# Kernel tuning notes

Measured on AMD Instinct MI355X. Metric: run time of the kernel, lower is better.

The kernel has to match this reference:

```python
import jax, jax.numpy as jnp
import numpy as np
import math

D_MODEL = 1024
N_HEAD = 16
D_FF = 4096
B, T, S = 2, 2048, 2048
LN_EPS = 1e-5


def _linear(x, w, b):
    # torch nn.Linear: y = x @ W.T + b, W: [out, in]
    return jnp.einsum('bsd,od->bso', x, w) + b


def _layer_norm(x, g, b):
    mu = jnp.mean(x, axis=-1, keepdims=True)
    var = jnp.var(x, axis=-1, keepdims=True)
    return (x - mu) * jax.lax.rsqrt(var + LN_EPS) * g + b


def _mha(xq, xkv, wq, bq, wk, bk, wv, bv, wo, bo, mask):
    Bq, Tq, D = xq.shape
    Tk = xkv.shape[1]
    dk = D // N_HEAD
    q = _linear(xq, wq, bq).reshape(Bq, Tq, N_HEAD, dk).transpose(0, 2, 1, 3)
    k = _linear(xkv, wk, bk).reshape(Bq, Tk, N_HEAD, dk).transpose(0, 2, 1, 3)
    v = _linear(xkv, wv, bv).reshape(Bq, Tk, N_HEAD, dk).transpose(0, 2, 1, 3)
    scores = jnp.einsum('bhqd,bhkd->bhqk', q, k) / math.sqrt(dk)
    if mask is not None:
        scores = jnp.where(mask == 0, jnp.asarray(-1e9, scores.dtype), scores)
    attn = jax.nn.softmax(scores, axis=-1)  # dropout is eval-mode identity
    out = jnp.einsum('bhqk,bhkd->bhqd', attn, v)
    out = out.transpose(0, 2, 1, 3).reshape(Bq, Tq, D)
    return _linear(out, wo, bo)


def setup_inputs() -> dict:
    key = jax.random.key(0)
    ks = jax.random.split(key, 20)
    sd = 0.02

    def w(k, shape):
        return (jax.random.normal(k, shape, dtype=jnp.float32) * sd)

    inp = {
        'x': jax.random.normal(ks[0], (B, T, D_MODEL), dtype=jnp.float32),
        'enc_output': jax.random.normal(ks[1], (B, S, D_MODEL), dtype=jnp.float32),
        # causal (future) mask for self-attention
        'tgt_mask': jnp.tril(jnp.ones((T, T), dtype=jnp.int32))[None, None, :, :].repeat(B, axis=0),
        # no source padding -> all ones
        'src_tgt_mask': jnp.ones((B, 1, T, S), dtype=jnp.int32),
        'sa_wq': w(ks[2], (D_MODEL, D_MODEL)), 'sa_bq': jnp.zeros((D_MODEL,), jnp.float32),
        'sa_wk': w(ks[3], (D_MODEL, D_MODEL)), 'sa_bk': jnp.zeros((D_MODEL,), jnp.float32),
        'sa_wv': w(ks[4], (D_MODEL, D_MODEL)), 'sa_bv': jnp.zeros((D_MODEL,), jnp.float32),
        'sa_wo': w(ks[5], (D_MODEL, D_MODEL)), 'sa_bo': jnp.zeros((D_MODEL,), jnp.float32),
        'ca_wq': w(ks[6], (D_MODEL, D_MODEL)), 'ca_bq': jnp.zeros((D_MODEL,), jnp.float32),
        'ca_wk': w(ks[7], (D_MODEL, D_MODEL)), 'ca_bk': jnp.zeros((D_MODEL,), jnp.float32),
        'ca_wv': w(ks[8], (D_MODEL, D_MODEL)), 'ca_bv': jnp.zeros((D_MODEL,), jnp.float32),
        'ca_wo': w(ks[9], (D_MODEL, D_MODEL)), 'ca_bo': jnp.zeros((D_MODEL,), jnp.float32),
        'ffn_w1': w(ks[10], (D_FF, D_MODEL)), 'ffn_b1': jnp.zeros((D_FF,), jnp.float32),
        'ffn_w2': w(ks[11], (D_MODEL, D_FF)), 'ffn_b2': jnp.zeros((D_MODEL,), jnp.float32),
        'ln1_g': jnp.ones((D_MODEL,), jnp.float32), 'ln1_b': jnp.zeros((D_MODEL,), jnp.float32),
        'ln2_g': jnp.ones((D_MODEL,), jnp.float32), 'ln2_b': jnp.zeros((D_MODEL,), jnp.float32),
        'ln3_g': jnp.ones((D_MODEL,), jnp.float32), 'ln3_b': jnp.zeros((D_MODEL,), jnp.float32),
    }
    return inp


def reference(x, enc_output, tgt_mask, src_tgt_mask,
              sa_wq, sa_bq, sa_wk, sa_bk, sa_wv, sa_bv, sa_wo, sa_bo,
              ca_wq, ca_bq, ca_wk, ca_bk, ca_wv, ca_bv, ca_wo, ca_bo,
              ffn_w1, ffn_b1, ffn_w2, ffn_b2,
              ln1_g, ln1_b, ln2_g, ln2_b, ln3_g, ln3_b):
    # masked self-attention + residual + LN
    a1 = _mha(x, x, sa_wq, sa_bq, sa_wk, sa_bk, sa_wv, sa_bv, sa_wo, sa_bo, tgt_mask)
    x = _layer_norm(x + a1, ln1_g, ln1_b)
    # cross-attention + residual + LN
    a2 = _mha(x, enc_output, ca_wq, ca_bq, ca_wk, ca_bk, ca_wv, ca_bv, ca_wo, ca_bo, src_tgt_mask)
    x = _layer_norm(x + a2, ln2_g, ln2_b)
    # FFN + residual + LN
    h = jax.nn.relu(_linear(x, ffn_w1, ffn_b1))
    f = _linear(h, ffn_w2, ffn_b2)
    x = _layer_norm(x + f, ln3_g, ln3_b)
    return x
```

## Files before the change

kernel.cpp:

```cpp
#include <hip/hip_runtime.h>
#include <stdint.h>

typedef uint16_t u16;
typedef __attribute__((ext_vector_type(8))) short short8;
typedef __attribute__((ext_vector_type(4))) short short4v;
typedef __attribute__((ext_vector_type(4))) float f32x4;
typedef __attribute__((ext_vector_type(2))) unsigned int u32x2;

#define GLB_AS __attribute__((address_space(1)))
#define LDS_AS __attribute__((address_space(3)))

__device__ __forceinline__ void gload_lds16(const void* g, void* l) {
  __builtin_amdgcn_global_load_lds((GLB_AS void*)(g), (LDS_AS void*)(l), 16, 0, 0);
}

__device__ __forceinline__ float bf2f(u16 u) {
  union { uint32_t i; float f; } v; v.i = ((uint32_t)u) << 16; return v.f;
}
__device__ __forceinline__ u16 f2bf(float f) {
  uint32_t x = __builtin_bit_cast(uint32_t, f);
  return (u16)((x + 0x7fffu + ((x >> 16) & 1u)) >> 16);
}
__device__ __forceinline__ uint32_t cvtpk(float lo, float hi) {
  uint32_t r;
  asm("v_cvt_pk_bf16_f32 %0, %1, %2" : "=v"(r) : "v"(lo), "v"(hi));
  return r;
}

struct CastJobs {
  const float* s[12];
  u16* d[12];
  int n[12];
};
__global__ __launch_bounds__(256) void cast_many(CastJobs j)
{
  const int job = blockIdx.y;
  const int i = (blockIdx.x * 256 + threadIdx.x) * 4;
  if (i >= j.n[job]) return;
  const float4 v = *(const float4*)(j.s[job] + i);
  short4v r;
  r[0] = (short)f2bf(v.x); r[1] = (short)f2bf(v.y);
  r[2] = (short)f2bf(v.z); r[3] = (short)f2bf(v.w);
  *(short4v*)(j.d[job] + i) = r;
}

__global__ __launch_bounds__(256) void vtrans(
    const u16* __restrict__ V, int vs, u16* __restrict__ Vt)
{
  __shared__ u16 tl[64][72];
  const int tid = threadIdx.x;
  const int b = blockIdx.z, h = blockIdx.y, t0 = blockIdx.x * 64;
#pragma unroll
  for (int it = 0; it < 2; ++it) {
    const int r = (tid >> 3) + it*32, c = (tid & 7) * 8;
    short8 vv = *(const short8*)(V + (size_t)(b*2048 + t0 + r)*vs + h*64 + c);
    *(short8*)(&tl[r][c]) = vv;
  }
  __syncthreads();
#pragma unroll
  for (int it = 0; it < 2; ++it) {
    const int d = (tid >> 3) + it*32, t8 = (tid & 7) * 8;
    short8 ov;
#pragma unroll
    for (int j = 0; j < 8; ++j) ov[j] = (short)tl[t8 + j][d];
    *(short8*)(Vt + ((size_t)((b*16 + h)*64 + d))*2048 + t0 + t8) = ov;
  }
}

template<int RELU, int NSEG, int BN>
__global__ __launch_bounds__(256) void gemm_bt(
    const u16* __restrict__ A, const u16* __restrict__ W,
    const float* __restrict__ b0, const float* __restrict__ b1,
    const float* __restrict__ b2, u16* __restrict__ Y,
    int M, int N, int K)
{
  __shared__ __attribute__((aligned(16))) u16 lA[128*64];
  __shared__ __attribute__((aligned(16))) u16 lB[BN*64];
  const int tid  = threadIdx.x;
  const int lane = tid & 63, wv = tid >> 6;
  constexpr int WM = (BN == 128) ? 64 : 32;
  constexpr int MI = WM / 16;
  constexpr int BRND = BN / 32;
  const int wm = (BN == 128) ? (wv >> 1) : wv;
  const int wn = (BN == 128) ? (wv & 1) : 0;
  const int l16 = lane & 15, l4 = lane >> 4;
  const int rswz = (l16 & 7) << 4;

  const int gx = gridDim.x;
  int flat = blockIdx.y * gx + blockIdx.x;
  flat = (flat & 7) * ((gx * gridDim.y) >> 3) + (flat >> 3);
  const int bx = (flat % gx) * BN, by = (flat / gx) * 128;

  const f32x4 fzero = {0.f, 0.f, 0.f, 0.f};
  f32x4 acc[MI][4];
#pragma unroll
  for (int i = 0; i < MI; ++i)
#pragma unroll
    for (int j = 0; j < 4; ++j) acc[i][j] = fzero;

  const int o = wv*1024 + lane*16;
  for (int k0 = 0; k0 < K; k0 += 64) {
#pragma unroll
    for (int r = 0; r < 4; ++r) {
      const int oo = r*4096 + o;
      const int row = oo >> 7;
      const int src = ((oo & 127) ^ ((row & 7) << 4)) >> 1;
      gload_lds16(A + (size_t)(by + row)*K + (k0 + src), (char*)lA + oo);
    }
#pragma unroll
    for (int r = 0; r < BRND; ++r) {
      const int oo = r*4096 + o;
      const int row = oo >> 7;
      const int src = ((oo & 127) ^ ((row & 7) << 4)) >> 1;
      gload_lds16(W + (size_t)(bx + row)*K + (k0 + src), (char*)lB + oo);
    }
    __syncthreads();
#pragma unroll
    for (int ks = 0; ks < 2; ++ks) {
      const int cb = (ks*64 + l4*16) ^ rswz;
      short8 af[MI], bfv[4];
#pragma unroll
      for (int i = 0; i < MI; ++i)
        af[i]  = *(const short8*)((const char*)lA + (wm*WM + i*16 + l16)*128 + cb);
#pragma unroll
      for (int j = 0; j < 4; ++j)
        bfv[j] = *(const short8*)((const char*)lB + (wn*64 + j*16 + l16)*128 + cb);
#pragma unroll
      for (int i = 0; i < MI; ++i)
#pragma unroll
        for (int j = 0; j < 4; ++j)
          acc[i][j] = __builtin_amdgcn_mfma_f32_16x16x32_bf16(af[i], bfv[j], acc[i][j], 0, 0, 0);
    }
    __syncthreads();
  }

#pragma unroll
  for (int j = 0; j < 4; ++j) {
    const int col = bx + wn*64 + j*16 + l16;
    float bv;
    if (NSEG == 1) bv = b0[col];
    else {
      const int seg = col >> 10, off = col & 1023;
      const float* bp = (seg == 0) ? b0 : ((seg == 1) ? b1 : b2);
      bv = bp[off];
    }
#pragma unroll
    for (int i = 0; i < MI; ++i) {
      const int r0 = by + wm*WM + i*16 + l4*4;
#pragma unroll
      for (int r = 0; r < 4; ++r) {
        float v = acc[i][j][r] + bv;
        if (RELU) v = v > 0.f ? v : 0.f;
        Y[(size_t)(r0 + r)*N + col] = f2bf(v);
      }
    }
  }
}

template<int CAUSAL, int QR>
__global__ __launch_bounds__(512, (QR == 16) ? 4 : 2) void attn_fwd(
    const u16* __restrict__ Q, int qs,
    const u16* __restrict__ K, int ks_,
    const u16* __restrict__ Vt, u16* __restrict__ O, int Tk)
{
  constexpr int NG = QR / 16;
  __shared__ __attribute__((aligned(16))) u16 lK[2][128*64];
  __shared__ __attribute__((aligned(16))) u16 lV[2][64*128];
  __shared__ __attribute__((aligned(16))) u16 lP[8][NG*1024];
  const int tid  = threadIdx.x;
  const int lane = tid & 63, wv = tid >> 6;
  const int l16 = lane & 15, l4 = lane >> 4;
  const int b = blockIdx.z, h = blockIdx.y;
  int strip;
  if (CAUSAL) {
    const int u = (blockIdx.x + blockIdx.z) & 15;
    strip = (u & 1) ? (15 - (u >> 1)) : (u >> 1);
  } else {
    strip = blockIdx.x;
  }
  const int Bq = strip * (8 * QR);
  const int qrow = Bq + wv*QR;

  short8 qf[NG][2];
#pragma unroll
  for (int g = 0; g < NG; ++g) {
    const u16* Qb = Q + (size_t)(b*2048 + qrow + g*16 + l16)*qs + h*64;
#pragma unroll
    for (int ks = 0; ks < 2; ++ks)
      qf[g][ks] = *(const short8*)(Qb + ks*32 + l4*8);
  }

  const f32x4 fzero = {0.f, 0.f, 0.f, 0.f};
  f32x4 accO[NG][4];
#pragma unroll
  for (int g = 0; g < NG; ++g)
#pragma unroll
    for (int i = 0; i < 4; ++i) accO[g][i] = fzero;
  float lrow[NG];
#pragma unroll
  for (int g = 0; g < NG; ++g) lrow[g] = 0.f;

  const int kend = CAUSAL ? (Bq + 8*QR) : Tk;
  const int nt = kend >> 7;
  const int qmax = qrow + QR - 1;
  const int srK = tid >> 3;
  const int scK = 8 * ((tid & 7) ^ (srK & 7));
  const int srV = tid >> 4;
  const int scV = 8 * ((tid & 15) ^ (srV & 7));
  const u16* KbG = K  + (size_t)(b*2048)*ks_ + h*64 + scK;
  const u16* VbG = Vt + ((size_t)((b*16 + h)*64 + srV))*2048 + scV;
  const int wvoff = (tid >> 6) * 1024;
  const int rswz = (l16 & 7) << 4;
  const float SCL = 0.18033688f;
  const int sbq = (lane & 48) + l4*4;

  char* const pbuf = (char*)lP + (tid >> 6) * (NG*2048);
  const int swzP = (l16 & 7) << 4;
  int wrA[4], rdA[2];
#pragma unroll
  for (int nf = 0; nf < 4; ++nf) wrA[nf] = l16*128 + ((nf*32 + l4*8) ^ swzP);
#pragma unroll
  for (int c = 0; c < 2; ++c)    rdA[c] = l16*128 + ((c*64 + l4*16) ^ swzP);

  auto readK = [&](int h2, int bb, short8 (&kf)[4][2]) {
#pragma unroll
    for (int nf = 0; nf < 4; ++nf) {
      const char* base = (const char*)lK[bb] + (h2*64 + nf*16 + l16)*128;
      kf[nf][0] = *(const short8*)(base + ((l4*16)      ^ rswz));
      kf[nf][1] = *(const short8*)(base + ((64 + l4*16) ^ rswz));
    }
  };

  auto compute64 = [&](int h2, int kvb, short8 (&kf)[4][2], int bb) {
#pragma unroll
    for (int g = 0; g < NG; ++g) {
      f32x4 sf[4];
      __builtin_amdgcn_s_setprio(1);
#pragma unroll
      for (int nf = 0; nf < 4; ++nf) {
        f32x4 s = fzero;
        s = __builtin_amdgcn_mfma_f32_16x16x32_bf16(kf[nf][0], qf[g][0], s, 0, 0, 0);
        s = __builtin_amdgcn_mfma_f32_16x16x32_bf16(kf[nf][1], qf[g][1], s, 0, 0, 0);
        sf[nf] = s;
      }
      __builtin_amdgcn_s_setprio(0);
      if (CAUSAL && (kvb + 63 > qrow + g*16)) {
        const int q = qrow + g*16 + l16;
#pragma unroll
        for (int nf = 0; nf < 4; ++nf)
#pragma unroll
          for (int r = 0; r < 4; ++r) {
            const int kv = kvb + nf*16 + l4*4 + r;
            if (kv > q) sf[nf][r] = -1e30f;
          }
      }
#pragma unroll
      for (int nf = 0; nf < 4; ++nf)
#pragma unroll
        for (int r = 0; r < 4; ++r)
          sf[nf][r] = exp2f(sf[nf][r] * SCL);
      float sm[4];
#pragma unroll
      for (int nf = 0; nf < 4; ++nf)
        sm[nf] = (sf[nf][0] + sf[nf][1]) + (sf[nf][2] + sf[nf][3]);
      lrow[g] += (sm[0] + sm[1]) + (sm[2] + sm[3]);
#pragma unroll
      for (int nf = 0; nf < 4; ++nf) {
        u32x2 w;
        w[0] = cvtpk(sf[nf][0], sf[nf][1]);
        w[1] = cvtpk(sf[nf][2], sf[nf][3]);
        *(u32x2*)(pbuf + g*2048 + wrA[nf]) = w;
      }
    }
#pragma unroll
    for (int c = 0; c < 2; ++c) {
      short8 pa[NG];
#pragma unroll
      for (int g = 0; g < NG; ++g)
        pa[g] = *(const short8*)(pbuf + g*2048 + rdA[c]);
      __builtin_amdgcn_s_setprio(1);
#pragma unroll
      for (int df = 0; df < 4; ++df) {
        const short8 vf = *(const short8*)((const char*)lV[bb] +
            (df*16 + l16)*256 + ((h2*128 + c*64 + l4*16) ^ rswz));
#pragma unroll
        for (int g = 0; g < NG; ++g)
          accO[g][df] = __builtin_amdgcn_mfma_f32_16x16x32_bf16(pa[g], vf, accO[g][df], 0, 0, 0);
      }
      __builtin_amdgcn_s_setprio(0);
    }
  };

#pragma unroll
  for (int r = 0; r < 2; ++r) {
    gload_lds16(KbG + (size_t)(r*64 + srK)*ks_, (char*)lK[0] + r*8192 + wvoff);
    gload_lds16(VbG + (size_t)(r*32)*2048,      (char*)lV[0] + r*8192 + wvoff);
  }

  for (int t = 0; t < nt; ++t) {
    const int bb = t & 1;
    const int kb = t << 7;
    __syncthreads();
    short8 kf[4][2];
    readK(0, bb, kf);
    if (t + 1 < nt) {
      const int kb2 = kb + 128;
#pragma unroll
      for (int r = 0; r < 2; ++r) {
        gload_lds16(KbG + (size_t)(kb2 + r*64 + srK)*ks_,
                    (char*)lK[bb^1] + r*8192 + wvoff);
        gload_lds16(VbG + (size_t)(r*32)*2048 + kb2,
                    (char*)lV[bb^1] + r*8192 + wvoff);
      }
    }
    compute64(0, kb, kf, bb);
    if (!CAUSAL || (kb + 64 <= qmax)) {
      readK(1, bb, kf);
      compute64(1, kb + 64, kf, bb);
    }
  }

#pragma unroll
  for (int g = 0; g < NG; ++g) {
    lrow[g] += __shfl_xor(lrow[g], 16);
    lrow[g] += __shfl_xor(lrow[g], 32);
    u16* Ob = O + (size_t)(b*2048 + qrow + g*16 + l4*4)*1024 + h*64;
#pragma unroll
    for (int r = 0; r < 4; ++r) {
      const float inv = 1.f / __shfl(lrow[g], sbq + r);
#pragma unroll
      for (int df = 0; df < 4; ++df)
        Ob[(size_t)r*1024 + df*16 + l16] = f2bf(accO[g][df][r] * inv);
    }
  }
}

template<int XF32, int OF32>
__global__ __launch_bounds__(256) void add_ln(
    const void* __restrict__ Xp, const u16* __restrict__ R,
    const float* __restrict__ G, const float* __restrict__ Bb,
    void* __restrict__ OUTp)
{
  const int row = blockIdx.x;
  const int tid = threadIdx.x;
  const size_t base = (size_t)row*1024 + tid*4;
  float xv[4];
  if (XF32) {
    const float4 t = *(const float4*)((const float*)Xp + base);
    xv[0] = t.x; xv[1] = t.y; xv[2] = t.z; xv[3] = t.w;
  } else {
    short4v t = *(const short4v*)((const u16*)Xp + base);
#pragma unroll
    for (int i = 0; i < 4; ++i) xv[i] = bf2f((u16)t[i]);
  }
  short4v rv = *(const short4v*)(R + base);
  float v[4], s = 0.f, s2 = 0.f;
#pragma unroll
  for (int i = 0; i < 4; ++i) {
    float t = xv[i] + bf2f((u16)rv[i]);
    v[i] = t; s += t; s2 += t*t;
  }
#pragma unroll
  for (int m = 1; m < 64; m <<= 1) { s += __shfl_xor(s, m); s2 += __shfl_xor(s2, m); }
  __shared__ float red[8];
  const int w = tid >> 6, lane = tid & 63;
  if (lane == 0) { red[w] = s; red[4 + w] = s2; }
  __syncthreads();
  s  = red[0] + red[1] + red[2] + red[3];
  s2 = red[4] + red[5] + red[6] + red[7];
  const float mu  = s * (1.f/1024.f);
  const float var = s2 * (1.f/1024.f) - mu*mu;
  const float rs  = rsqrtf(var + 1e-5f);
  if (OF32) {
    float4 ov;
    ov.x = (v[0]-mu)*rs*G[tid*4+0] + Bb[tid*4+0];
    ov.y = (v[1]-mu)*rs*G[tid*4+1] + Bb[tid*4+1];
    ov.z = (v[2]-mu)*rs*G[tid*4+2] + Bb[tid*4+2];
    ov.w = (v[3]-mu)*rs*G[tid*4+3] + Bb[tid*4+3];
    *(float4*)((float*)OUTp + base) = ov;
  } else {
    short4v ov;
#pragma unroll
    for (int i = 0; i < 4; ++i)
      ov[i] = (short)f2bf((v[i] - mu)*rs*G[tid*4+i] + Bb[tid*4+i]);
    *(short4v*)((u16*)OUTp + base) = ov;
  }
}

extern "C" void kernel_launch(void* const* d_in, const int* in_sizes, int n_in,
                              void* d_out, int out_size, void* d_ws, size_t ws_size,
                              hipStream_t stream)
{
  (void)in_sizes; (void)n_in; (void)out_size; (void)ws_size;
  const float* x    = (const float*)d_in[0];
  const float* enc  = (const float*)d_in[1];
  const float* sa_wq = (const float*)d_in[4];  const float* sa_bq = (const float*)d_in[5];
  const float* sa_wk = (const float*)d_in[6];  const float* sa_bk = (const float*)d_in[7];
  const float* sa_wv = (const float*)d_in[8];  const float* sa_bv = (const float*)d_in[9];
  const float* sa_wo = (const float*)d_in[10]; const float* sa_bo = (const float*)d_in[11];
  const float* ca_wq = (const float*)d_in[12]; const float* ca_bq = (const float*)d_in[13];
  const float* ca_wk = (const float*)d_in[14]; const float* ca_bk = (const float*)d_in[15];
  const float* ca_wv = (const float*)d_in[16]; const float* ca_bv = (const float*)d_in[17];
  const float* ca_wo = (const float*)d_in[18]; const float* ca_bo = (const float*)d_in[19];
  const float* w1 = (const float*)d_in[20];    const float* b1 = (const float*)d_in[21];
  const float* w2 = (const float*)d_in[22];    const float* b2 = (const float*)d_in[23];
  const float* ln1g = (const float*)d_in[24];  const float* ln1b = (const float*)d_in[25];
  const float* ln2g = (const float*)d_in[26];  const float* ln2b = (const float*)d_in[27];
  const float* ln3g = (const float*)d_in[28];  const float* ln3b = (const float*)d_in[29];
  float* out = (float*)d_out;

  char* ws = (char*)d_ws;
  const size_t MB = 1024*1024;
  u16* xb   = (u16*)(ws);
  u16* encb = (u16*)(ws + 8*MB);
  u16* wsab = (u16*)(ws + 16*MB);
  u16* wcab = (u16*)(ws + 24*MB);
  u16* x1   = (u16*)(ws + 32*MB);
  u16* ao   = (u16*)(ws + 40*MB);
  u16* tmp  = (u16*)(ws + 48*MB);
  u16* vt   = (u16*)(ws + 56*MB);
  u16* qkv  = (u16*)(ws + 64*MB);
  u16* kvb  = (u16*)(ws + 88*MB);
  u16* x2   = xb;
  u16* hb   = qkv;
  u16* w1b  = encb;
  u16* w2b  = vt;

  const int NW = 1024*1024;
  const int NX = 4096*1024;
  dim3 blk(256);

  {
    CastJobs cj{};
    cj.s[0] = x;     cj.d[0] = xb;           cj.n[0] = NX;
    cj.s[1] = enc;   cj.d[1] = encb;         cj.n[1] = NX;
    cj.s[2] = sa_wq; cj.d[2] = wsab + 0*NW;  cj.n[2] = NW;
    cj.s[3] = sa_wk; cj.d[3] = wsab + 1*NW;  cj.n[3] = NW;
    cj.s[4] = sa_wv; cj.d[4] = wsab + 2*NW;  cj.n[4] = NW;
    cj.s[5] = sa_wo; cj.d[5] = wsab + 3*NW;  cj.n[5] = NW;
    cj.s[6] = ca_wq; cj.d[6] = wcab + 0*NW;  cj.n[6] = NW;
    cj.s[7] = ca_wk; cj.d[7] = wcab + 1*NW;  cj.n[7] = NW;
    cj.s[8] = ca_wv; cj.d[8] = wcab + 2*NW;  cj.n[8] = NW;
    cj.s[9] = ca_wo; cj.d[9] = wcab + 3*NW;  cj.n[9] = NW;
    cast_many<<<dim3(NX/1024, 10), blk, 0, stream>>>(cj);
  }

  const int M = 4096;
  dim3 gN64(16, 32);
  dim3 gQKV(24, 32);
  dim3 gKV(16, 32);
  dim3 gF1(32, 32);
  dim3 gAself(16, 16, 2);
  dim3 gAcross(8, 16, 2);
  dim3 gT(32, 16, 2);
  dim3 blk512(512);

  gemm_bt<0,3,128><<<gQKV, blk, 0, stream>>>(xb, wsab, sa_bq, sa_bk, sa_bv, qkv, M, 3072, 1024);
  vtrans<<<gT, blk, 0, stream>>>(qkv + 2048, 3072, vt);
  attn_fwd<1,16><<<gAself, blk512, 0, stream>>>(qkv, 3072, qkv + 1024, 3072, vt, ao, 2048);
  gemm_bt<0,1,64><<<gN64, blk, 0, stream>>>(ao, wsab + 3*NW, sa_bo, sa_bo, sa_bo, tmp, M, 1024, 1024);
  add_ln<1,0><<<4096, blk, 0, stream>>>(x, tmp, ln1g, ln1b, x1);

  gemm_bt<0,1,64><<<gN64, blk, 0, stream>>>(x1, wcab + 0*NW, ca_bq, ca_bq, ca_bq, qkv, M, 1024, 1024);
  gemm_bt<0,2,128><<<gKV, blk, 0, stream>>>(encb, wcab + 1*NW, ca_bk, ca_bv, ca_bv, kvb, M, 2048, 1024);
  vtrans<<<gT, blk, 0, stream>>>(kvb + 1024, 2048, vt);
  attn_fwd<0,32><<<gAcross, blk512, 0, stream>>>(qkv, 1024, kvb, 2048, vt, ao, 2048);
  {
    CastJobs cj{};
    cj.s[0] = w1; cj.d[0] = w1b; cj.n[0] = NX;
    cj.s[1] = w2; cj.d[1] = w2b; cj.n[1] = NX;
    cast_many<<<dim3(NX/1024, 2), blk, 0, stream>>>(cj);
  }
  gemm_bt<0,1,64><<<gN64, blk, 0, stream>>>(ao, wcab + 3*NW, ca_bo, ca_bo, ca_bo, tmp, M, 1024, 1024);
  add_ln<0,0><<<4096, blk, 0, stream>>>(x1, tmp, ln2g, ln2b, x2);

  gemm_bt<1,1,128><<<gF1, blk, 0, stream>>>(x2, w1b, b1, b1, b1, hb, M, 4096, 1024);
  gemm_bt<0,1,64><<<gN64, blk, 0, stream>>>(hb, w2b, b2, b2, b2, tmp, M, 1024, 4096);
  add_ln<0,1><<<4096, blk, 0, stream>>>(x2, tmp, ln3g, ln3b, out);
}
```

Baseline: 370.3 us.

## Double-buffer GEMM LDS tiles and use 16-row attention tiles for cross-attention

The GEMM now keeps two LDS buffers for the A and B tiles. It issues the global-to-LDS loads for the next K tile after reading the current tile's fragments into registers, so memory transfer overlaps with the MFMA work and one barrier per iteration is removed. Cross-attention switches from the 32-row template with an 8-block grid dimension to the 16-row template with a 16-block grid, giving twice as many blocks. The double buffering doubles LDS use per block, which may lower occupancy. The single barrier relies on the fragment reads completing before the next stage overwrites the other buffer.

Result: faster. 328.1 us (-11.4%).

```diff
diff --git a/kernel.cpp b/kernel.cpp
--- a/kernel.cpp
+++ b/kernel.cpp
@@ -74,8 +74,8 @@
     const float* __restrict__ b2, u16* __restrict__ Y,
     int M, int N, int K)
 {
-  __shared__ __attribute__((aligned(16))) u16 lA[128*64];
-  __shared__ __attribute__((aligned(16))) u16 lB[BN*64];
+  __shared__ __attribute__((aligned(16))) u16 lA[2][128*64];
+  __shared__ __attribute__((aligned(16))) u16 lB[2][BN*64];
   const int tid  = threadIdx.x;
   const int lane = tid & 63, wv = tid >> 6;
   constexpr int WM = (BN == 128) ? 64 : 32;
@@ -99,39 +99,48 @@
     for (int j = 0; j < 4; ++j) acc[i][j] = fzero;
 
   const int o = wv*1024 + lane*16;
-  for (int k0 = 0; k0 < K; k0 += 64) {
+
+  auto stage = [&](int k0, int buf) {
 #pragma unroll
     for (int r = 0; r < 4; ++r) {
       const int oo = r*4096 + o;
       const int row = oo >> 7;
       const int src = ((oo & 127) ^ ((row & 7) << 4)) >> 1;
-      gload_lds16(A + (size_t)(by + row)*K + (k0 + src), (char*)lA + oo);
+      gload_lds16(A + (size_t)(by + row)*K + (k0 + src), (char*)lA[buf] + oo);
     }
 #pragma unroll
     for (int r = 0; r < BRND; ++r) {
       const int oo = r*4096 + o;
       const int row = oo >> 7;
       const int src = ((oo & 127) ^ ((row & 7) << 4)) >> 1;
-      gload_lds16(W + (size_t)(bx + row)*K + (k0 + src), (char*)lB + oo);
-    }
+      gload_lds16(W + (size_t)(bx + row)*K + (k0 + src), (char*)lB[buf] + oo);
+    }
+  };
+
+  stage(0, 0);
+  const int KT = K >> 6;
+  for (int kt = 0; kt < KT; ++kt) {
+    const int cur = kt & 1;
     __syncthreads();
+    short8 af[2][MI], bfv[2][4];
 #pragma unroll
     for (int ks = 0; ks < 2; ++ks) {
       const int cb = (ks*64 + l4*16) ^ rswz;
-      short8 af[MI], bfv[4];
 #pragma unroll
       for (int i = 0; i < MI; ++i)
-        af[i]  = *(const short8*)((const char*)lA + (wm*WM + i*16 + l16)*128 + cb);
+        af[ks][i]  = *(const short8*)((const char*)lA[cur] + (wm*WM + i*16 + l16)*128 + cb);
 #pragma unroll
       for (int j = 0; j < 4; ++j)
-        bfv[j] = *(const short8*)((const char*)lB + (wn*64 + j*16 + l16)*128 + cb);
+        bfv[ks][j] = *(const short8*)((const char*)lB[cur] + (wn*64 + j*16 + l16)*128 + cb);
+    }
+    if (kt + 1 < KT) stage((kt + 1) << 6, cur ^ 1);
+#pragma unroll
+    for (int ks = 0; ks < 2; ++ks)
 #pragma unroll
       for (int i = 0; i < MI; ++i)
 #pragma unroll
         for (int j = 0; j < 4; ++j)
-          acc[i][j] = __builtin_amdgcn_mfma_f32_16x16x32_bf16(af[i], bfv[j], acc[i][j], 0, 0, 0);
-    }
-    __syncthreads();
+          acc[i][j] = __builtin_amdgcn_mfma_f32_16x16x32_bf16(af[ks][i], bfv[ks][j], acc[i][j], 0, 0, 0);
   }
 
 #pragma unroll
@@ -450,21 +459,20 @@
   dim3 gQKV(24, 32);
   dim3 gKV(16, 32);
   dim3 gF1(32, 32);
-  dim3 gAself(16, 16, 2);
-  dim3 gAcross(8, 16, 2);
+  dim3 gAttn(16, 16, 2);
   dim3 gT(32, 16, 2);
   dim3 blk512(512);
 
   gemm_bt<0,3,128><<<gQKV, blk, 0, stream>>>(xb, wsab, sa_bq, sa_bk, sa_bv, qkv, M, 3072, 1024);
   vtrans<<<gT, blk, 0, stream>>>(qkv + 2048, 3072, vt);
-  attn_fwd<1,16><<<gAself, blk512, 0, stream>>>(qkv, 3072, qkv + 1024, 3072, vt, ao, 2048);
+  attn_fwd<1,16><<<gAttn, blk512, 0, stream>>>(qkv, 3072, qkv + 1024, 3072, vt, ao, 2048);
   gemm_bt<0,1,64><<<gN64, blk, 0, stream>>>(ao, wsab + 3*NW, sa_bo, sa_bo, sa_bo, tmp, M, 1024, 1024);
   add_ln<1,0><<<4096, blk, 0, stream>>>(x, tmp, ln1g, ln1b, x1);
 
   gemm_bt<0,1,64><<<gN64, blk, 0, stream>>>(x1, wcab + 0*NW, ca_bq, ca_bq, ca_bq, qkv, M, 1024, 1024);
   gemm_bt<0,2,128><<<gKV, blk, 0, stream>>>(encb, wcab + 1*NW, ca_bk, ca_bv, ca_bv, kvb, M, 2048, 1024);
   vtrans<<<gT, blk, 0, stream>>>(kvb + 1024, 2048, vt);
-  attn_fwd<0,32><<<gAcross, blk512, 0, stream>>>(qkv, 1024, kvb, 2048, vt, ao, 2048);
+  attn_fwd<0,16><<<gAttn, blk512, 0, stream>>>(qkv, 1024, kvb, 2048, vt, ao, 2048);
   {
     CastJobs cj{};
     cj.s[0] = w1; cj.d[0] = w1b; cj.n[0] = NX;
```
